# Kernel tuning notes

Measured on AMD Instinct MI355X. Metric: run time of the kernel, lower is better.

## Reference

```python
import jax, jax.numpy as jnp
import numpy as np

N = 100000      # num nodes
E = 3200000     # num edges
F = 128         # feature dim (in == out, required by final in-place copy)
U = 1000        # num_users


def gcn_conv(x, edge_index, W, b):
    """PyG GCNConv: symmetric-normalized adjacency with self-loops.
    out = D^{-1/2} (A + I) D^{-1/2} X W + b
    """
    xw = x @ W                                   # [N, F]
    src, dst = edge_index[0], edge_index[1]
    # in-degree including the self-loop (+1)
    deg = jax.ops.segment_sum(jnp.ones((E,), x.dtype), dst, num_segments=N) + 1.0
    inv_sqrt = jax.lax.rsqrt(deg)                # [N]
    coef = inv_sqrt[src] * inv_sqrt[dst]         # [E]
    agg = jax.ops.segment_sum(xw[src] * coef[:, None], dst, num_segments=N)
    # self-loop contribution: norm_ii = inv_sqrt[i]^2
    return agg + xw * (inv_sqrt * inv_sqrt)[:, None] + b


def setup_inputs() -> dict:
    key = jax.random.key(0)
    k1, k2, k3, k4, k5, k6 = jax.random.split(key, 6)
    x = jax.random.normal(k1, (N, F), dtype=jnp.float32)
    edge_index = jax.random.randint(k2, (2, E), 0, N, dtype=jnp.int64)
    s = 1.0 / np.sqrt(F)
    W1 = jax.random.normal(k3, (F, F), dtype=jnp.float32) * s
    b1 = jnp.zeros((F,), dtype=jnp.float32)
    W2 = jax.random.normal(k4, (F, F), dtype=jnp.float32) * s
    b2 = jnp.zeros((F,), dtype=jnp.float32)
    return {"x": x, "edge_index": edge_index, "W1": W1, "b1": b1, "W2": W2, "b2": b2}


def reference(x, edge_index, W1, b1, W2, b2):
    # eval mode: dropout(p=0.5, training=False) is identity; detach is a no-op in fwd
    h = jax.nn.elu(gcn_conv(x, edge_index, W1, b1))
    h = jax.nn.elu(gcn_conv(h, edge_index, W2, b2))
    # x[num_users:] = movie_features  -> movie rows restored to original input
    return jnp.concatenate([h[:U], x[U:]], axis=0)
```

## Files before the change

kernel.cpp:

```cpp
#include <hip/hip_runtime.h>


#define F_DIM 128
#define U_USERS 1000
#define SCAN_CHUNK 1024
#define NFCAP 48000
#define NCHUNK 3
#define SBIN 40960
#define SW (SBIN / 2)
#define PSLICE 85
#define BMW 3136
#define SMEM_BYTES 32768

using f16x8 = __attribute__((ext_vector_type(8))) _Float16;
using f16x2 = __attribute__((ext_vector_type(2))) _Float16;
using f32x4 = __attribute__((ext_vector_type(4))) float;

__global__ __launch_bounds__(1024) void hist_kernel(const int* __restrict__ src,
                                                    const int* __restrict__ dst,
                                                    unsigned int* __restrict__ partial,
                                                    int* __restrict__ fr, int E, int n) {
    __shared__ unsigned int h[SW];
    int tid = threadIdx.x;
    int c = blockIdx.x % NCHUNK;
    int p = blockIdx.x / NCHUNK;
    for (int i = tid; i < SW; i += 1024) h[i] = 0u;
    __syncthreads();

    int lo = c * SBIN;
    int hi = lo + SBIN;
    int len = (E + PSLICE - 1) / PSLICE;
    int base = p * len;
    int end = min(E, base + len);
    int e = base + tid * 4;
    for (; e + 3 < end; e += 4096) {
        int4 dv = *(const int4*)(dst + e);
#pragma unroll
        for (int i = 0; i < 4; ++i) {
            int d = ((const int*)&dv)[i];
            if ((unsigned)d < (unsigned)n) {
                if (d >= lo && d < hi) {
                    int local = d - lo;
                    atomicAdd(&h[local >> 1], 1u << ((local & 1) << 4));
                }
                if (c == 0 && d < U_USERS) {
                    int s = src[e + i];
                    if ((unsigned)s < (unsigned)n) fr[s] = 1;
                }
            }
        }
    }
    for (; e < end; ++e) {
        int d = dst[e];
        if ((unsigned)d < (unsigned)n) {
            if (d >= lo && d < hi) {
                int local = d - lo;
                atomicAdd(&h[local >> 1], 1u << ((local & 1) << 4));
            }
            if (c == 0 && d < U_USERS) {
                int s = src[e];
                if ((unsigned)s < (unsigned)n) fr[s] = 1;
            }
        }
    }
    __syncthreads();
    unsigned int* outp = partial + ((size_t)(c * PSLICE + p)) * SW;
    for (int i = tid; i < SW; i += 1024) outp[i] = h[i];
}

__global__ void reduce_prep_kernel(const unsigned int* __restrict__ partial,
                                   float* __restrict__ inv, int* __restrict__ fr,
                                   int* __restrict__ degF,
                                   unsigned int* __restrict__ bitsG, int n) {
    int t = blockIdx.x * blockDim.x + threadIdx.x;
    if (t >= NCHUNK * SW) return;
    int c = t / SW, w = t % SW;
    unsigned int a0 = 0, a1 = 0;
    const unsigned int* basep = partial + (size_t)c * PSLICE * SW + w;
#pragma unroll 5
    for (int p = 0; p < PSLICE; ++p) {
        unsigned int v = basep[(size_t)p * SW];
        a0 += v & 0xFFFFu;
        a1 += v >> 16;
    }
    int i0 = c * SBIN + 2 * w;
    unsigned int pair = 0u;
#pragma unroll
    for (int k = 0; k < 2; ++k) {
        int i = i0 + k;
        unsigned int dg = k ? a1 : a0;
        if (i < n) {
            inv[i] = rsqrtf((float)dg + 1.0f);
            bool isfr = (i < U_USERS) || (fr[i] != 0);
            if (i < U_USERS) fr[i] = 1;
            degF[i] = isfr ? (int)dg : 0;
            if (isfr) pair |= (1u << k);
        }
    }
    if (pair) atomicOr(&bitsG[i0 >> 5], pair << (i0 & 31));
}

__global__ void scan_reduce2_kernel(const int* __restrict__ dA, const int* __restrict__ dB,
                                    int* __restrict__ pA, int* __restrict__ pB, int n) {
    __shared__ int sdata[256];
    int b = blockIdx.x, t = threadIdx.x;
    int base = b * SCAN_CHUNK;
    int sumA = 0, sumB = 0;
#pragma unroll
    for (int i = 0; i < 4; ++i) {
        int idx = base + t + 256 * i;
        if (idx < n) { sumA += dA[idx]; sumB += dB[idx]; }
    }
    sdata[t] = sumA; __syncthreads();
    for (int s = 128; s > 0; s >>= 1) { if (t < s) sdata[t] += sdata[t + s]; __syncthreads(); }
    if (t == 0) pA[b] = sdata[0];
    __syncthreads();
    sdata[t] = sumB; __syncthreads();
    for (int s = 128; s > 0; s >>= 1) { if (t < s) sdata[t] += sdata[t + s]; __syncthreads(); }
    if (t == 0) pB[b] = sdata[0];
}

__global__ void scan_partials2_kernel(int* __restrict__ pA, int* __restrict__ pB, int nb) {
    int wv = threadIdx.x >> 6, lane = threadIdx.x & 63;
    int* p = wv ? pB : pA;
    int i0 = lane * 2, i1 = lane * 2 + 1;
    int v0 = (i0 < nb) ? p[i0] : 0;
    int v1 = (i1 < nb) ? p[i1] : 0;
    int sum = v0 + v1;
    int incl = sum;
    for (int ofs = 1; ofs < 64; ofs <<= 1) {
        int t = __shfl_up(incl, ofs);
        if (lane >= ofs) incl += t;
    }
    int run = incl - sum;
    if (i0 < nb) p[i0] = run;
    if (i1 < nb) p[i1] = run + v0;
}

__global__ void scan_final2_kernel(const int* __restrict__ dA, const int* __restrict__ pA,
                                   int* __restrict__ rp,
                                   const int* __restrict__ dB, const int* __restrict__ pB,
                                   int* __restrict__ remap,
                                   int* __restrict__ flist, int* __restrict__ nf_dev, int n) {
    __shared__ int sthread[256];
    int b = blockIdx.x, t = threadIdx.x;
    int base = b * SCAN_CHUNK;
    {
        int v[4]; int sum = 0;
#pragma unroll
        for (int i = 0; i < 4; ++i) { int idx = base + 4 * t + i; v[i] = (idx < n) ? dA[idx] : 0; sum += v[i]; }
        sthread[t] = sum; __syncthreads();
        for (int ofs = 1; ofs < 256; ofs <<= 1) {
            int val = (t >= ofs) ? sthread[t - ofs] : 0;
            __syncthreads(); sthread[t] += val; __syncthreads();
        }
        int run = sthread[t] - sum + pA[b];
#pragma unroll
        for (int i = 0; i < 4; ++i) { int idx = base + 4 * t + i; if (idx < n) rp[idx] = run; run += v[i]; }
        __syncthreads();
    }
    {
        int v[4]; int sum = 0;
#pragma unroll
        for (int i = 0; i < 4; ++i) { int idx = base + 4 * t + i; v[i] = (idx < n) ? dB[idx] : 0; sum += v[i]; }
        sthread[t] = sum; __syncthreads();
        for (int ofs = 1; ofs < 256; ofs <<= 1) {
            int val = (t >= ofs) ? sthread[t - ofs] : 0;
            __syncthreads(); sthread[t] += val; __syncthreads();
        }
        int run = sthread[t] - sum + pB[b];
#pragma unroll
        for (int i = 0; i < 4; ++i) {
            int idx = base + 4 * t + i;
            if (idx < n) {
                remap[idx] = run;
                if (v[i] && run < NFCAP) flist[run] = idx;
                if (idx == n - 1) *nf_dev = min(run + v[i], NFCAP);
            }
            run += v[i];
        }
    }
}

__device__ __forceinline__ void fill_csr_body(const int* __restrict__ src,
                                              const int* __restrict__ dst,
                                              const unsigned int* __restrict__ bitsG,
                                              int* __restrict__ rp, int* __restrict__ col,
                                              int E, int n, int fblk,
                                              unsigned char* smem) {
    unsigned int* bm = (unsigned int*)smem;
    int tid = threadIdx.x;
    int nw = (n + 31) >> 5;
    for (int i = tid; i < nw; i += 256) bm[i] = bitsG[i];
    __syncthreads();

    int t = fblk * 256 + tid;
    int e0 = t * 4;
    if (e0 + 3 < E) {
        int4 dv = *(const int4*)(dst + e0);
        int4 sv = *(const int4*)(src + e0);
        const int* dp = (const int*)&dv;
        const int* sp = (const int*)&sv;
        bool f[4];
#pragma unroll
        for (int i = 0; i < 4; ++i) {
            int d = dp[i];
            f[i] = ((unsigned)d < (unsigned)n) && ((unsigned)sp[i] < (unsigned)n)
                   && ((bm[d >> 5] >> (d & 31)) & 1u);
        }
        int pos[4];
#pragma unroll
        for (int i = 0; i < 4; ++i) {
            pos[i] = -1;
            if (f[i]) pos[i] = atomicAdd(&rp[dp[i]], 1);
        }
#pragma unroll
        for (int i = 0; i < 4; ++i) {
            if (f[i] && (unsigned)pos[i] < (unsigned)E) col[pos[i]] = sp[i];
        }
    } else {
        for (int e = e0; e < E; ++e) {
            int d = dst[e], s = src[e];
            if ((unsigned)d < (unsigned)n && (unsigned)s < (unsigned)n &&
                ((bm[d >> 5] >> (d & 31)) & 1u)) {
                int pos = atomicAdd(&rp[d], 1);
                if ((unsigned)pos < (unsigned)E) col[pos] = s;
            }
        }
    }
}

__device__ __forceinline__ void stage_wt(const float* __restrict__ W, _Float16* Wt, int tid) {
#pragma unroll
    for (int i = 0; i < 8; ++i) {
        int j = tid + 256 * i;
        int nr = j & 127;
        int k8 = j >> 7;
        f16x8 v;
#pragma unroll
        for (int kk = 0; kk < 8; ++kk)
            v[kk] = (_Float16)W[(k8 * 8 + kk) * F_DIM + nr];
        *(f16x8*)&Wt[nr * F_DIM + ((k8 ^ (nr & 15)) * 8)] = v;
    }
}

__device__ __forceinline__ void gemm_mfma_body(const float* __restrict__ X,
                                               const float* __restrict__ W,
                                               _Float16* __restrict__ outh,
                                               float* __restrict__ pout,
                                               int nrows, int rowBase,
                                               unsigned char* smem) {
    _Float16* Wt = (_Float16*)smem;
    int tid = threadIdx.x;
    stage_wt(W, Wt, tid);
    __syncthreads();

    int w = tid >> 6;
    int lane = tid & 63;
    int m = lane & 15;
    int quad = lane >> 4;
    int row = rowBase + w * 16 + m;
    bool rv = row < nrows;

    f16x8 a0, a1, a2, a3;
    {
        const float* xr = X + (size_t)row * F_DIM;
        float* pr = (pout != nullptr && rv && row >= U_USERS)
                        ? pout + (size_t)row * F_DIM : nullptr;
#pragma unroll
        for (int kc = 0; kc < 4; ++kc) {
            float4 lo = make_float4(0.f, 0.f, 0.f, 0.f);
            float4 hi = lo;
            if (rv) {
                lo = ((const float4*)(xr + kc * 32 + quad * 8))[0];
                hi = ((const float4*)(xr + kc * 32 + quad * 8))[1];
            }
            if (pr) {
                ((float4*)(pr + kc * 32 + quad * 8))[0] = lo;
                ((float4*)(pr + kc * 32 + quad * 8))[1] = hi;
            }
            f16x8 av;
            av[0] = (_Float16)lo.x; av[1] = (_Float16)lo.y;
            av[2] = (_Float16)lo.z; av[3] = (_Float16)lo.w;
            av[4] = (_Float16)hi.x; av[5] = (_Float16)hi.y;
            av[6] = (_Float16)hi.z; av[7] = (_Float16)hi.w;
            if (kc == 0) a0 = av; else if (kc == 1) a1 = av;
            else if (kc == 2) a2 = av; else a3 = av;
        }
    }

    f32x4 acc[8];
#pragma unroll
    for (int i = 0; i < 8; ++i) acc[i] = (f32x4){0.f, 0.f, 0.f, 0.f};

#pragma unroll
    for (int kc = 0; kc < 4; ++kc) {
        f16x8 a = (kc == 0) ? a0 : (kc == 1) ? a1 : (kc == 2) ? a2 : a3;
#pragma unroll
        for (int ct = 0; ct < 8; ++ct) {
            f16x8 b = *(const f16x8*)&Wt[(ct * 16 + m) * F_DIM +
                                         (((kc * 4 + quad) ^ m) * 8)];
            acc[ct] = __builtin_amdgcn_mfma_f32_16x16x32_f16(a, b, acc[ct], 0, 0, 0);
        }
    }

#pragma unroll
    for (int ct = 0; ct < 8; ++ct) {
#pragma unroll
        for (int reg = 0; reg < 4; ++reg) {
            int r = rowBase + w * 16 + quad * 4 + reg;
            if (r < nrows)
                outh[(size_t)r * F_DIM + ct * 16 + m] = (_Float16)acc[ct][reg];
        }
    }
}

__device__ __forceinline__ void gemm_mfma_body_h(const _Float16* __restrict__ Xh,
                                                 const float* __restrict__ W,
                                                 _Float16* __restrict__ outh,
                                                 int nrows, int rowBase,
                                                 unsigned char* smem) {
    _Float16* Wt = (_Float16*)smem;
    int tid = threadIdx.x;
    stage_wt(W, Wt, tid);
    __syncthreads();

    int w = tid >> 6;
    int lane = tid & 63;
    int m = lane & 15;
    int quad = lane >> 4;
    int row = rowBase + w * 16 + m;
    const _Float16* xr = Xh + (size_t)row * F_DIM;

    f32x4 acc[8];
#pragma unroll
    for (int i = 0; i < 8; ++i) acc[i] = (f32x4){0.f, 0.f, 0.f, 0.f};

#pragma unroll
    for (int kc = 0; kc < 4; ++kc) {
        f16x8 a = *(const f16x8*)(xr + kc * 32 + quad * 8);
#pragma unroll
        for (int ct = 0; ct < 8; ++ct) {
            f16x8 b = *(const f16x8*)&Wt[(ct * 16 + m) * F_DIM +
                                         (((kc * 4 + quad) ^ m) * 8)];
            acc[ct] = __builtin_amdgcn_mfma_f32_16x16x32_f16(a, b, acc[ct], 0, 0, 0);
        }
    }

#pragma unroll
    for (int ct = 0; ct < 8; ++ct) {
#pragma unroll
        for (int reg = 0; reg < 4; ++reg) {
            int r = rowBase + w * 16 + quad * 4 + reg;
            if (r < nrows)
                outh[(size_t)r * F_DIM + ct * 16 + m] = (_Float16)acc[ct][reg];
        }
    }
}

__global__ __launch_bounds__(256) void gemm_fill_kernel(const float* __restrict__ X,
                                                        const float* __restrict__ W,
                                                        _Float16* __restrict__ outh,
                                                        float* __restrict__ pout, int nrows,
                                                        int gemmBlocks, int totalBlocks,
                                                        const int* __restrict__ src,
                                                        const int* __restrict__ dst,
                                                        const unsigned int* __restrict__ bitsG,
                                                        int* __restrict__ rp,
                                                        int* __restrict__ col, int E, int n) {
    __shared__ __align__(16) unsigned char smem[SMEM_BYTES];
    int b = blockIdx.x;
    long long g = gemmBlocks, T = totalBlocks;
    int before = (int)((long long)b * g / T);
    int after  = (int)(((long long)b + 1) * g / T);
    if (after > before) {
        gemm_mfma_body(X, W, outh, pout, nrows, before * 64, smem);
    } else {
        fill_csr_body(src, dst, bitsG, rp, col, E, n, b - before, smem);
    }
}

__global__ __launch_bounds__(256) void gemm_f16_dyn_kernel(const _Float16* __restrict__ Xh,
                                                           const float* __restrict__ W,
                                                           _Float16* __restrict__ outh,
                                                           const int* __restrict__ nrows_p) {
    __shared__ __align__(16) unsigned char smem[SMEM_BYTES];
    int nrows = *nrows_p;
    int rowBase = blockIdx.x * 64;
    if (rowBase >= nrows) return;
    gemm_mfma_body_h(Xh, W, outh, nrows, rowBase, smem);
}

__global__ __launch_bounds__(256) void gather_l1_kernel(const _Float16* __restrict__ xwh,
                                                        const float* __restrict__ inv,
                                                        const int* __restrict__ rp,
                                                        const int* __restrict__ col,
                                                        const int* __restrict__ flist,
                                                        const int* __restrict__ nf_p,
                                                        const float* __restrict__ b,
                                                        _Float16* __restrict__ h1c) {
    int ci = blockIdx.x * 4 + (threadIdx.x >> 6);
    if (ci >= *nf_p) return;
    int lane = threadIdx.x & 63;
    int node = flist[ci];
    int start = (node == 0) ? 0 : rp[node - 1];
    int end = rp[node];

    float accx = 0.f, accy = 0.f;
    for (int base = start; base < end; base += 64) {
        int j = base + lane;
        int s_l = 0; float c_l = 0.f;
        if (j < end) { s_l = col[j]; c_l = inv[s_l]; }
        int cnt = min(64, end - base);
        int i = 0;
        for (; i + 8 <= cnt; i += 8) {
            int ss[8]; float ff[8]; f16x2 vv[8];
#pragma unroll
            for (int u = 0; u < 8; ++u) { ss[u] = __shfl(s_l, i + u); ff[u] = __shfl(c_l, i + u); }
#pragma unroll
            for (int u = 0; u < 8; ++u) vv[u] = ((const f16x2*)(xwh + (size_t)ss[u] * F_DIM))[lane];
#pragma unroll
            for (int u = 0; u < 8; ++u) { accx += (float)vv[u][0] * ff[u]; accy += (float)vv[u][1] * ff[u]; }
        }
        for (; i + 4 <= cnt; i += 4) {
            int ss[4]; float ff[4]; f16x2 vv[4];
#pragma unroll
            for (int u = 0; u < 4; ++u) { ss[u] = __shfl(s_l, i + u); ff[u] = __shfl(c_l, i + u); }
#pragma unroll
            for (int u = 0; u < 4; ++u) vv[u] = ((const f16x2*)(xwh + (size_t)ss[u] * F_DIM))[lane];
#pragma unroll
            for (int u = 0; u < 4; ++u) { accx += (float)vv[u][0] * ff[u]; accy += (float)vv[u][1] * ff[u]; }
        }
        for (; i < cnt; ++i) {
            int s0 = __shfl(s_l, i); float f0 = __shfl(c_l, i);
            f16x2 v0 = ((const f16x2*)(xwh + (size_t)s0 * F_DIM))[lane];
            accx += (float)v0[0] * f0;
            accy += (float)v0[1] * f0;
        }
    }

    float ivd = inv[node];
    f16x2 self = ((const f16x2*)(xwh + (size_t)node * F_DIM))[lane];
    float vx = accx * ivd + (float)self[0] * ivd * ivd + b[lane * 2];
    float vy = accy * ivd + (float)self[1] * ivd * ivd + b[lane * 2 + 1];
    vx = vx > 0.f ? vx : expf(vx) - 1.f;
    vy = vy > 0.f ? vy : expf(vy) - 1.f;
    f16x2 o; o[0] = (_Float16)vx; o[1] = (_Float16)vy;
    ((f16x2*)(h1c + (size_t)ci * F_DIM))[lane] = o;
}

__global__ __launch_bounds__(256) void gather_l2_kernel(const _Float16* __restrict__ xwc,
                                                        const float* __restrict__ inv,
                                                        const int* __restrict__ rp,
                                                        const int* __restrict__ col,
                                                        const int* __restrict__ remap,
                                                        const float* __restrict__ b,
                                                        float* __restrict__ out) {
    int node = blockIdx.x * 4 + (threadIdx.x >> 6);
    if (node >= U_USERS) return;
    int lane = threadIdx.x & 63;
    int start = (node == 0) ? 0 : rp[node - 1];
    int end = rp[node];

    float accx = 0.f, accy = 0.f;
    for (int base = start; base < end; base += 64) {
        int j = base + lane;
        int r_l = 0; float c_l = 0.f;
        if (j < end) { int s = col[j]; c_l = inv[s]; r_l = remap[s]; }
        int cnt = min(64, end - base);
        int i = 0;
        for (; i + 8 <= cnt; i += 8) {
            int rr[8]; float ff[8]; f16x2 vv[8];
#pragma unroll
            for (int u = 0; u < 8; ++u) { rr[u] = __shfl(r_l, i + u); ff[u] = __shfl(c_l, i + u); }
#pragma unroll
            for (int u = 0; u < 8; ++u) vv[u] = ((const f16x2*)(xwc + (size_t)rr[u] * F_DIM))[lane];
#pragma unroll
            for (int u = 0; u < 8; ++u) { accx += (float)vv[u][0] * ff[u]; accy += (float)vv[u][1] * ff[u]; }
        }
        for (; i + 4 <= cnt; i += 4) {
            int rr[4]; float ff[4]; f16x2 vv[4];
#pragma unroll
            for (int u = 0; u < 4; ++u) { rr[u] = __shfl(r_l, i + u); ff[u] = __shfl(c_l, i + u); }
#pragma unroll
            for (int u = 0; u < 4; ++u) vv[u] = ((const f16x2*)(xwc + (size_t)rr[u] * F_DIM))[lane];
#pragma unroll
            for (int u = 0; u < 4; ++u) { accx += (float)vv[u][0] * ff[u]; accy += (float)vv[u][1] * ff[u]; }
        }
        for (; i < cnt; ++i) {
            int r0 = __shfl(r_l, i); float f0 = __shfl(c_l, i);
            f16x2 v0 = ((const f16x2*)(xwc + (size_t)r0 * F_DIM))[lane];
            accx += (float)v0[0] * f0;
            accy += (float)v0[1] * f0;
        }
    }

    float ivd = inv[node];
    f16x2 self = ((const f16x2*)(xwc + (size_t)node * F_DIM))[lane];
    float vx = accx * ivd + (float)self[0] * ivd * ivd + b[lane * 2];
    float vy = accy * ivd + (float)self[1] * ivd * ivd + b[lane * 2 + 1];
    vx = vx > 0.f ? vx : expf(vx) - 1.f;
    vy = vy > 0.f ? vy : expf(vy) - 1.f;
    ((float2*)(out + (size_t)node * F_DIM))[lane] = make_float2(vx, vy);
}

extern "C" void kernel_launch(void* const* d_in, const int* in_sizes, int n_in,
                              void* d_out, int out_size, void* d_ws, size_t ws_size,
                              hipStream_t stream) {
    const float* x  = (const float*)d_in[0];
    const int*   ei = (const int*)d_in[1];
    const float* W1 = (const float*)d_in[2];
    const float* b1 = (const float*)d_in[3];
    const float* W2 = (const float*)d_in[4];
    const float* b2 = (const float*)d_in[5];
    float* out = (float*)d_out;

    int n = in_sizes[0] / F_DIM;
    int E = in_sizes[1] / 2;
    const int* srcI = ei;
    const int* dstI = ei + E;

    _Float16* xwh = (_Float16*)d_ws;
    _Float16* h1c = xwh + (size_t)n * F_DIM;
    float* inv   = (float*)(h1c + (size_t)NFCAP * F_DIM * 2);
    int* fr      = (int*)(inv + n);
    int* degF    = fr + n;
    int* remap   = degF + n;
    int* rp      = remap + n;
    int* flist   = rp + n;
    int* pA      = flist + NFCAP;
    int* pB      = pA + 1024;
    int* nf_dev  = pB + 1024;
    int* col     = nf_dev + 16;
    unsigned int* partialH = (unsigned int*)(col + E);
    unsigned int* bitsG = partialH + (size_t)NCHUNK * PSLICE * SW;

    int nb = (n + SCAN_CHUNK - 1) / SCAN_CHUNK;

    hipMemsetAsync(fr, 0, (size_t)n * sizeof(int), stream);
    hipMemsetAsync(bitsG, 0, (size_t)BMW * sizeof(unsigned int), stream);

    hist_kernel<<<NCHUNK * PSLICE, 1024, 0, stream>>>(srcI, dstI, partialH, fr, E, n);
    reduce_prep_kernel<<<(NCHUNK * SW + 255) / 256, 256, 0, stream>>>(partialH, inv, fr, degF, bitsG, n);

    scan_reduce2_kernel<<<nb, 256, 0, stream>>>(degF, fr, pA, pB, n);
    scan_partials2_kernel<<<1, 128, 0, stream>>>(pA, pB, nb);
    scan_final2_kernel<<<nb, 256, 0, stream>>>(degF, pA, rp, fr, pB, remap, flist, nf_dev, n);

    int fillBlocks = (E / 4 + 255) / 256;
    int gemmBlocks = (n + 63) / 64;
    gemm_fill_kernel<<<fillBlocks + gemmBlocks, 256, 0, stream>>>(
        x, W1, xwh, out, n, gemmBlocks, fillBlocks + gemmBlocks,
        srcI, dstI, bitsG, rp, col, E, n);

    gather_l1_kernel<<<(NFCAP + 3) / 4, 256, 0, stream>>>(xwh, inv, rp, col, flist, nf_dev, b1, h1c);

    gemm_f16_dyn_kernel<<<(NFCAP + 63) / 64, 256, 0, stream>>>(h1c, W2, xwh, nf_dev);
    gather_l2_kernel<<<(U_USERS + 3) / 4, 256, 0, stream>>>(xwh, inv, rp, col, remap, b2, out);
}
```

Measured before the change: 279.5 us.

## Fuse degree reduction and both prefix scans into one decoupled-lookback kernel

Replaces the reduce_prep kernel and the three-kernel two-array scan with a single prep_scan kernel. Each 1024-thread block reduces the histogram partials for 2048 nodes, writes inv and the frontier bitmap, and does a packed 64-bit scan of degree and frontier flag together. Blocks chain their prefixes through a global descriptor lookback with spin-waits. Two memsets become one zero kernel, and the degF/pA/pB buffers are removed. This cuts launches and intermediate global traffic, but the inter-block spin relies on earlier blocks being resident and makes the scan serial across only 49 blocks.

```diff
diff --git a/kernel.cpp b/kernel.cpp
--- a/kernel.cpp
+++ b/kernel.cpp
@@ -3,7 +3,6 @@
 
 #define F_DIM 128
 #define U_USERS 1000
-#define SCAN_CHUNK 1024
 #define NFCAP 48000
 #define NCHUNK 3
 #define SBIN 40960
@@ -11,10 +10,21 @@
 #define PSLICE 85
 #define BMW 3136
 #define SMEM_BYTES 32768
+#define NBPS 49
 
 using f16x8 = __attribute__((ext_vector_type(8))) _Float16;
 using f16x2 = __attribute__((ext_vector_type(2))) _Float16;
 using f32x4 = __attribute__((ext_vector_type(4))) float;
+
+__global__ __launch_bounds__(256) void zero_kernel(int* __restrict__ fr,
+                                                   unsigned long long* __restrict__ desc,
+                                                   int n) {
+    int t = blockIdx.x * 256 + threadIdx.x;
+    int n4 = n >> 2;
+    if (t < n4) ((int4*)fr)[t] = make_int4(0, 0, 0, 0);
+    if (t < (n & 3)) fr[(n & ~3) + t] = 0;
+    if (t < NBPS) desc[t] = 0ull;
+}
 
 __global__ __launch_bounds__(1024) void hist_kernel(const int* __restrict__ src,
                                                     const int* __restrict__ dst,
@@ -68,118 +78,84 @@
     for (int i = tid; i < SW; i += 1024) outp[i] = h[i];
 }
 
-__global__ void reduce_prep_kernel(const unsigned int* __restrict__ partial,
-                                   float* __restrict__ inv, int* __restrict__ fr,
-                                   int* __restrict__ degF,
-                                   unsigned int* __restrict__ bitsG, int n) {
-    int t = blockIdx.x * blockDim.x + threadIdx.x;
-    if (t >= NCHUNK * SW) return;
-    int c = t / SW, w = t % SW;
-    unsigned int a0 = 0, a1 = 0;
-    const unsigned int* basep = partial + (size_t)c * PSLICE * SW + w;
+__global__ __launch_bounds__(1024) void prep_scan_kernel(
+    const unsigned int* __restrict__ partial, const int* __restrict__ fr,
+    float* __restrict__ inv, int* __restrict__ rp, int* __restrict__ remap,
+    int* __restrict__ flist, int* __restrict__ nf_dev,
+    unsigned int* __restrict__ bitsG, unsigned long long* __restrict__ desc, int n) {
+    __shared__ unsigned long long ss[1024];
+    __shared__ unsigned int bmw[64];
+    __shared__ unsigned long long spre;
+    int b = blockIdx.x, t = threadIdx.x;
+    int i0 = b * 2048 + t * 2;
+
+    unsigned a0 = 0, a1 = 0;
+    {
+        int c = i0 / SBIN;
+        int w = (i0 - c * SBIN) >> 1;
+        const unsigned int* bp = partial + (size_t)c * PSLICE * SW + w;
 #pragma unroll 5
-    for (int p = 0; p < PSLICE; ++p) {
-        unsigned int v = basep[(size_t)p * SW];
-        a0 += v & 0xFFFFu;
-        a1 += v >> 16;
-    }
-    int i0 = c * SBIN + 2 * w;
-    unsigned int pair = 0u;
-#pragma unroll
-    for (int k = 0; k < 2; ++k) {
-        int i = i0 + k;
-        unsigned int dg = k ? a1 : a0;
-        if (i < n) {
-            inv[i] = rsqrtf((float)dg + 1.0f);
-            bool isfr = (i < U_USERS) || (fr[i] != 0);
-            if (i < U_USERS) fr[i] = 1;
-            degF[i] = isfr ? (int)dg : 0;
-            if (isfr) pair |= (1u << k);
-        }
-    }
-    if (pair) atomicOr(&bitsG[i0 >> 5], pair << (i0 & 31));
-}
-
-__global__ void scan_reduce2_kernel(const int* __restrict__ dA, const int* __restrict__ dB,
-                                    int* __restrict__ pA, int* __restrict__ pB, int n) {
-    __shared__ int sdata[256];
-    int b = blockIdx.x, t = threadIdx.x;
-    int base = b * SCAN_CHUNK;
-    int sumA = 0, sumB = 0;
-#pragma unroll
-    for (int i = 0; i < 4; ++i) {
-        int idx = base + t + 256 * i;
-        if (idx < n) { sumA += dA[idx]; sumB += dB[idx]; }
-    }
-    sdata[t] = sumA; __syncthreads();
-    for (int s = 128; s > 0; s >>= 1) { if (t < s) sdata[t] += sdata[t + s]; __syncthreads(); }
-    if (t == 0) pA[b] = sdata[0];
-    __syncthreads();
-    sdata[t] = sumB; __syncthreads();
-    for (int s = 128; s > 0; s >>= 1) { if (t < s) sdata[t] += sdata[t + s]; __syncthreads(); }
-    if (t == 0) pB[b] = sdata[0];
-}
-
-__global__ void scan_partials2_kernel(int* __restrict__ pA, int* __restrict__ pB, int nb) {
-    int wv = threadIdx.x >> 6, lane = threadIdx.x & 63;
-    int* p = wv ? pB : pA;
-    int i0 = lane * 2, i1 = lane * 2 + 1;
-    int v0 = (i0 < nb) ? p[i0] : 0;
-    int v1 = (i1 < nb) ? p[i1] : 0;
-    int sum = v0 + v1;
-    int incl = sum;
-    for (int ofs = 1; ofs < 64; ofs <<= 1) {
-        int t = __shfl_up(incl, ofs);
-        if (lane >= ofs) incl += t;
-    }
-    int run = incl - sum;
-    if (i0 < nb) p[i0] = run;
-    if (i1 < nb) p[i1] = run + v0;
-}
-
-__global__ void scan_final2_kernel(const int* __restrict__ dA, const int* __restrict__ pA,
-                                   int* __restrict__ rp,
-                                   const int* __restrict__ dB, const int* __restrict__ pB,
-                                   int* __restrict__ remap,
-                                   int* __restrict__ flist, int* __restrict__ nf_dev, int n) {
-    __shared__ int sthread[256];
-    int b = blockIdx.x, t = threadIdx.x;
-    int base = b * SCAN_CHUNK;
-    {
-        int v[4]; int sum = 0;
-#pragma unroll
-        for (int i = 0; i < 4; ++i) { int idx = base + 4 * t + i; v[i] = (idx < n) ? dA[idx] : 0; sum += v[i]; }
-        sthread[t] = sum; __syncthreads();
-        for (int ofs = 1; ofs < 256; ofs <<= 1) {
-            int val = (t >= ofs) ? sthread[t - ofs] : 0;
-            __syncthreads(); sthread[t] += val; __syncthreads();
-        }
-        int run = sthread[t] - sum + pA[b];
-#pragma unroll
-        for (int i = 0; i < 4; ++i) { int idx = base + 4 * t + i; if (idx < n) rp[idx] = run; run += v[i]; }
-        __syncthreads();
-    }
-    {
-        int v[4]; int sum = 0;
-#pragma unroll
-        for (int i = 0; i < 4; ++i) { int idx = base + 4 * t + i; v[i] = (idx < n) ? dB[idx] : 0; sum += v[i]; }
-        sthread[t] = sum; __syncthreads();
-        for (int ofs = 1; ofs < 256; ofs <<= 1) {
-            int val = (t >= ofs) ? sthread[t - ofs] : 0;
-            __syncthreads(); sthread[t] += val; __syncthreads();
-        }
-        int run = sthread[t] - sum + pB[b];
-#pragma unroll
-        for (int i = 0; i < 4; ++i) {
-            int idx = base + 4 * t + i;
-            if (idx < n) {
-                remap[idx] = run;
-                if (v[i] && run < NFCAP) flist[run] = idx;
-                if (idx == n - 1) *nf_dev = min(run + v[i], NFCAP);
-            }
-            run += v[i];
-        }
-    }
+        for (int p = 0; p < PSLICE; ++p) {
+            unsigned v = bp[(size_t)p * SW];
+            a0 += v & 0xFFFFu; a1 += v >> 16;
+        }
+    }
+    bool in0 = i0 < n, in1 = i0 + 1 < n;
+    int fv0 = 0, fv1 = 0;
+    if (in1) { int2 f2 = *(const int2*)(fr + i0); fv0 = f2.x; fv1 = f2.y; }
+    else if (in0) fv0 = fr[i0];
+    int isf0 = (in0 && ((i0 < U_USERS) || fv0)) ? 1 : 0;
+    int isf1 = (in1 && ((i0 + 1 < U_USERS) || fv1)) ? 1 : 0;
+    unsigned d0 = isf0 ? a0 : 0u, d1 = isf1 ? a1 : 0u;
+
+    if (in1) *(float2*)(inv + i0) = make_float2(rsqrtf((float)a0 + 1.f),
+                                                rsqrtf((float)a1 + 1.f));
+    else if (in0) inv[i0] = rsqrtf((float)a0 + 1.f);
+
+    if (t < 64) bmw[t] = 0u;
+    __syncthreads();
+    unsigned pbits = (unsigned)isf0 | ((unsigned)isf1 << 1);
+    if (pbits) atomicOr(&bmw[(t * 2) >> 5], pbits << ((t * 2) & 31));
+    __syncthreads();
+    if (t < 64) bitsG[b * 64 + t] = bmw[t];
+
+    unsigned long long myv = ((unsigned long long)(d0 + d1) << 20) |
+                             (unsigned)(isf0 + isf1);
+    ss[t] = myv;
+    __syncthreads();
+    for (int ofs = 1; ofs < 1024; ofs <<= 1) {
+        unsigned long long v = (t >= ofs) ? ss[t - ofs] : 0ull;
+        __syncthreads(); ss[t] += v; __syncthreads();
+    }
+    unsigned long long total = ss[1023];
+
+    if (t == 0) atomicExch(&desc[b], (total << 1) | 1ull);
+    if (t < 64) {
+        int pblk = b - 1 - t;
+        unsigned long long v = 0ull;
+        if (pblk >= 0) {
+            unsigned long long d;
+            do { d = atomicAdd(&desc[pblk], 0ull); } while (!(d & 1ull));
+            v = d >> 1;
+        }
+#pragma unroll
+        for (int o = 32; o > 0; o >>= 1) v += __shfl_down(v, o);
+        if (t == 0) spre = v;
+    }
+    __syncthreads();
+
+    unsigned long long ex = spre + ss[t] - myv;
+    int rp0 = (int)(ex >> 20), rm0 = (int)(ex & 0xFFFFFu);
+    unsigned long long ex1 = ex + ((((unsigned long long)d0) << 20) | (unsigned)isf0);
+    int rp1 = (int)(ex1 >> 20), rm1 = (int)(ex1 & 0xFFFFFu);
+    if (in1) {
+        *(int2*)(rp + i0) = make_int2(rp0, rp1);
+        *(int2*)(remap + i0) = make_int2(rm0, rm1);
+    } else if (in0) { rp[i0] = rp0; remap[i0] = rm0; }
+    if (isf0 && rm0 < NFCAP) flist[rm0] = i0;
+    if (isf1 && rm1 < NFCAP) flist[rm1] = i0 + 1;
+    if (in0 && i0 == n - 1) *nf_dev = min(rp0 * 0 + rm0 + isf0, NFCAP);
+    if (in1 && i0 + 1 == n - 1) *nf_dev = min(rm1 + isf1, NFCAP);
 }
 
 __device__ __forceinline__ void fill_csr_body(const int* __restrict__ src,
@@ -522,30 +498,23 @@
 
     _Float16* xwh = (_Float16*)d_ws;
     _Float16* h1c = xwh + (size_t)n * F_DIM;
-    float* inv   = (float*)(h1c + (size_t)NFCAP * F_DIM * 2);
+    float* inv   = (float*)(h1c + (size_t)NFCAP * F_DIM);
     int* fr      = (int*)(inv + n);
-    int* degF    = fr + n;
-    int* remap   = degF + n;
+    int* remap   = fr + n;
     int* rp      = remap + n;
     int* flist   = rp + n;
-    int* pA      = flist + NFCAP;
-    int* pB      = pA + 1024;
-    int* nf_dev  = pB + 1024;
+    int* nf_dev  = flist + NFCAP;
     int* col     = nf_dev + 16;
     unsigned int* partialH = (unsigned int*)(col + E);
     unsigned int* bitsG = partialH + (size_t)NCHUNK * PSLICE * SW;
-
-    int nb = (n + SCAN_CHUNK - 1) / SCAN_CHUNK;
-
-    hipMemsetAsync(fr, 0, (size_t)n * sizeof(int), stream);
-    hipMemsetAsync(bitsG, 0, (size_t)BMW * sizeof(unsigned int), stream);
+    unsigned long long* desc = (unsigned long long*)(bitsG + BMW);
+
+    zero_kernel<<<(n / 4 + 255) / 256, 256, 0, stream>>>(fr, desc, n);
 
     hist_kernel<<<NCHUNK * PSLICE, 1024, 0, stream>>>(srcI, dstI, partialH, fr, E, n);
-    reduce_prep_kernel<<<(NCHUNK * SW + 255) / 256, 256, 0, stream>>>(partialH, inv, fr, degF, bitsG, n);
-
-    scan_reduce2_kernel<<<nb, 256, 0, stream>>>(degF, fr, pA, pB, n);
-    scan_partials2_kernel<<<1, 128, 0, stream>>>(pA, pB, nb);
-    scan_final2_kernel<<<nb, 256, 0, stream>>>(degF, pA, rp, fr, pB, remap, flist, nf_dev, n);
+
+    prep_scan_kernel<<<NBPS, 1024, 0, stream>>>(partialH, fr, inv, rp, remap,
+                                                flist, nf_dev, bitsG, desc, n);
 
     int fillBlocks = (E / 4 + 255) / 256;
     int gemmBlocks = (n + 63) / 64;
```

New measurement: 268.9 us. -3.8%, faster.
